# Optimization experiments

Hardware: AMD Instinct MI355X
Metric: run time of the kernel (lower is better)

Reference implementation:

```python
import jax, jax.numpy as jnp
import numpy as np
import math

FACTOR = 180.0 / math.pi  # radians -> degrees


def setup_inputs() -> dict:
    key = jax.random.key(0)
    inputs = jax.random.normal(key, (128, 65536, 3), dtype=jnp.float32)
    return {"inputs": inputs}


def reference(inputs) -> jnp.ndarray:
    # inputs: [B, L, 3]; fully vectorized version of the nested map_fn
    x = inputs[..., 0]
    y = inputs[..., 1]
    z = inputs[..., 2]
    pi = jnp.float32(math.pi)
    phi = (jnp.clip(x, -1.0, 1.0) + 1.0) * pi / 2.0
    n = jnp.sqrt(y * y + z * z)
    psi = jnp.arccos(y / n)
    psi = jnp.where(z < 0, -psi, psi)
    factor = jnp.float32(FACTOR)
    return jnp.stack([-phi * factor, psi * factor], axis=-1)  # [B, L, 2]
```

## Files before the change

### kernel.cpp

```cpp
#include <hip/hip_runtime.h>
#include <math.h>


#define DEG_PER_RAD 57.29577951308232f

__device__ __forceinline__ void point_math(float x, float y, float z,
                                           float& o0, float& o1) {
    float xc = fminf(fmaxf(x, -1.0f), 1.0f);
    o0 = -90.0f * (xc + 1.0f);
    float n = sqrtf(y * y + z * z);
    float psi = acosf(y / n);
    psi = (z < 0.0f) ? -psi : psi;
    o1 = psi * DEG_PER_RAD;
}

__global__ __launch_bounds__(256) void cil_kernel(const float4* __restrict__ in4,
                                                  float4* __restrict__ out4,
                                                  int n_quads) {
    int i = blockIdx.x * blockDim.x + threadIdx.x;
    if (i >= n_quads) return;

    float4 f0 = in4[3 * i + 0];
    float4 f1 = in4[3 * i + 1];
    float4 f2 = in4[3 * i + 2];

    float o0x, o0y, o1x, o1y, o2x, o2y, o3x, o3y;
    point_math(f0.x, f0.y, f0.z, o0x, o0y);
    point_math(f0.w, f1.x, f1.y, o1x, o1y);
    point_math(f1.z, f1.w, f2.x, o2x, o2y);
    point_math(f2.y, f2.z, f2.w, o3x, o3y);

    out4[2 * i + 0] = make_float4(o0x, o0y, o1x, o1y);
    out4[2 * i + 1] = make_float4(o2x, o2y, o3x, o3y);
}

__global__ void cil_tail_kernel(const float* __restrict__ in,
                                float* __restrict__ out,
                                int start_point, int n_points) {
    int p = start_point + blockIdx.x * blockDim.x + threadIdx.x;
    if (p >= n_points) return;
    float x = in[3 * p + 0];
    float y = in[3 * p + 1];
    float z = in[3 * p + 2];
    float o0, o1;
    point_math(x, y, z, o0, o1);
    out[2 * p + 0] = o0;
    out[2 * p + 1] = o1;
}

extern "C" void kernel_launch(void* const* d_in, const int* in_sizes, int n_in,
                              void* d_out, int out_size, void* d_ws, size_t ws_size,
                              hipStream_t stream) {
    const float* in = (const float*)d_in[0];
    float* out = (float*)d_out;
    int n_points = in_sizes[0] / 3;
    int n_quads = n_points / 4;

    if (n_quads > 0) {
        int block = 256;
        int grid = (n_quads + block - 1) / block;
        cil_kernel<<<grid, block, 0, stream>>>((const float4*)in, (float4*)out, n_quads);
    }
    int tail_start = n_quads * 4;
    int tail = n_points - tail_start;
    if (tail > 0) {
        cil_tail_kernel<<<1, 64, 0, stream>>>(in, out, tail_start, n_points);
    }
}
```

Before: 162.7 us.

## Stage loads and stores through LDS for fully coalesced vector access

Each block now loads 1024 points with consecutive-thread float4 loads into shared memory, computes per-thread from LDS, then writes outputs back through LDS with coalesced nontemporal float4 stores. This replaces the strided 3-float4-per-thread load and 2-float4 store pattern, which spreads each wavefront's accesses across more cache lines per instruction. It adds two barriers and LDS traffic, and strided LDS reads (stride 12 floats) may cause bank conflicts.

```diff
diff --git a/kernel.cpp b/kernel.cpp
--- a/kernel.cpp
+++ b/kernel.cpp
@@ -3,6 +3,8 @@
 
 
 #define DEG_PER_RAD 57.29577951308232f
+
+typedef float vfloat4 __attribute__((ext_vector_type(4)));
 
 __device__ __forceinline__ void point_math(float x, float y, float z,
                                            float& o0, float& o1) {
@@ -14,24 +16,42 @@
     o1 = psi * DEG_PER_RAD;
 }
 
-__global__ __launch_bounds__(256) void cil_kernel(const float4* __restrict__ in4,
-                                                  float4* __restrict__ out4,
-                                                  int n_quads) {
-    int i = blockIdx.x * blockDim.x + threadIdx.x;
-    if (i >= n_quads) return;
+__global__ __launch_bounds__(256) void cil_kernel(const vfloat4* __restrict__ in4,
+                                                  vfloat4* __restrict__ out4) {
+    __shared__ float lds_in[3072];
+    __shared__ float lds_out[2048];
 
-    float4 f0 = in4[3 * i + 0];
-    float4 f1 = in4[3 * i + 1];
-    float4 f2 = in4[3 * i + 2];
+    const int b = blockIdx.x;
+    const int t = threadIdx.x;
 
-    float o0x, o0y, o1x, o1y, o2x, o2y, o3x, o3y;
-    point_math(f0.x, f0.y, f0.z, o0x, o0y);
-    point_math(f0.w, f1.x, f1.y, o1x, o1y);
-    point_math(f1.z, f1.w, f2.x, o2x, o2y);
-    point_math(f2.y, f2.z, f2.w, o3x, o3y);
+    const vfloat4* src = in4 + (size_t)b * 768;
+    vfloat4 v0 = src[t];
+    vfloat4 v1 = src[t + 256];
+    vfloat4 v2 = src[t + 512];
+    vfloat4* li4 = (vfloat4*)lds_in;
+    li4[t]       = v0;
+    li4[t + 256] = v1;
+    li4[t + 512] = v2;
+    __syncthreads();
 
-    out4[2 * i + 0] = make_float4(o0x, o0y, o1x, o1y);
-    out4[2 * i + 1] = make_float4(o2x, o2y, o3x, o3y);
+    float p[12];
+#pragma unroll
+    for (int k = 0; k < 12; ++k) p[k] = lds_in[12 * t + k];
+
+    float o[8];
+#pragma unroll
+    for (int q = 0; q < 4; ++q)
+        point_math(p[3 * q], p[3 * q + 1], p[3 * q + 2], o[2 * q], o[2 * q + 1]);
+
+#pragma unroll
+    for (int k = 0; k < 8; ++k) lds_out[8 * t + k] = o[k];
+    __syncthreads();
+
+    vfloat4* dst = out4 + (size_t)b * 512;
+    vfloat4 w0 = ((vfloat4*)lds_out)[t];
+    vfloat4 w1 = ((vfloat4*)lds_out)[t + 256];
+    __builtin_nontemporal_store(w0, &dst[t]);
+    __builtin_nontemporal_store(w1, &dst[t + 256]);
 }
 
 __global__ void cil_tail_kernel(const float* __restrict__ in,
@@ -53,17 +73,18 @@
                               hipStream_t stream) {
     const float* in = (const float*)d_in[0];
     float* out = (float*)d_out;
-    int n_points = in_sizes[0] / 3;
-    int n_quads = n_points / 4;
+    const int n_points = in_sizes[0] / 3;
+    const int n_full_blocks = n_points / 1024;
 
-    if (n_quads > 0) {
+    if (n_full_blocks > 0) {
+        cil_kernel<<<n_full_blocks, 256, 0, stream>>>((const vfloat4*)in,
+                                                      (vfloat4*)out);
+    }
+    const int tail_start = n_full_blocks * 1024;
+    const int tail = n_points - tail_start;
+    if (tail > 0) {
         int block = 256;
-        int grid = (n_quads + block - 1) / block;
-        cil_kernel<<<grid, block, 0, stream>>>((const float4*)in, (float4*)out, n_quads);
-    }
-    int tail_start = n_quads * 4;
-    int tail = n_points - tail_start;
-    if (tail > 0) {
-        cil_tail_kernel<<<1, 64, 0, stream>>>(in, out, tail_start, n_points);
+        int grid = (tail + block - 1) / block;
+        cil_tail_kernel<<<grid, block, 0, stream>>>(in, out, tail_start, n_points);
     }
 }
```

After: 161.7 us, median of 2. No clear change (-0.6%).
